# Performance work log

Measured on AMD Instinct MI355X. Metric: run time of the kernel, lower is better.

Reference implementation:

```python
import jax, jax.numpy as jnp
import numpy as np

DIM = 4096
DIM_OUTS = (4096, 4096, 4096)
R = 8
SCALE = 1.0  # alpha defaults to r -> alpha/r = 1


def setup_inputs() -> dict:
    key = jax.random.key(0)
    ks = jax.random.split(key, 1 + len(DIM_OUTS))
    x = jax.random.normal(ks[0], (4, 4096, DIM), dtype=jnp.float32)
    # A ~ randn, B ~ zeros per torch init; use small randn for B so grads/outputs are nontrivial? 
    # Faithful to module init: B = zeros. Keep zeros.
    As = [jax.random.normal(ks[1 + i], (DIM, R), dtype=jnp.float32) for i in range(len(DIM_OUTS))]
    Bs = [jnp.zeros((R, d), dtype=jnp.float32) for d in DIM_OUTS]
    return {
        "x": x,
        "A0": As[0], "B0": Bs[0],
        "A1": As[1], "B1": Bs[1],
        "A2": As[2], "B2": Bs[2],
    }


def reference(x, A0, B0, A1, B1, A2, B2):
    # Faithful math: x @ concat([A_i @ B_i * scale], axis=-1)
    # Efficient form: compute (x @ A_i) @ B_i * scale per LoRA, then concat.
    # Same Rs allow stacking into one batched low-rank chain.
    A = jnp.stack([A0, A1, A2])          # [L, dim, r]
    B = jnp.stack([B0, B1, B2])          # [L, r, dim_out]
    xa = jnp.einsum('bsd,ldr->lbsr', x, A)   # [L, B, S, r]
    out = jnp.einsum('lbsr,lro->lbso', xa, B) * SCALE  # [L, B, S, dim_out]
    # concat along last dim in lora order
    L, Bb, S, O = out.shape
    return jnp.moveaxis(out, 0, 2).reshape(Bb, S, L * O)
```

## Files before the change

### kernel.cpp

```cpp
#include <hip/hip_runtime.h>


#define DIM       4096
#define M_ROWS    16384
#define NLORA     3
#define RANK      8
#define NC        24
#define OUT_COLS  12288

#define KC             512
#define ROWS_PER_WAVE  4
#define ROWS_PER_BLOCK 16

__launch_bounds__(256, 2)
__global__ void lora_xa_kernel(const float* __restrict__ x,
                               const float* __restrict__ A0,
                               const float* __restrict__ A1,
                               const float* __restrict__ A2,
                               float* __restrict__ xa) {
  __shared__ float At[NC][KC];

  const int tid  = threadIdx.x;
  const int lane = tid & 63;
  const int wave = tid >> 6;
  const int row0 = blockIdx.x * ROWS_PER_BLOCK + wave * ROWS_PER_WAVE;

  float acc[ROWS_PER_WAVE][NC];
#pragma unroll
  for (int r = 0; r < ROWS_PER_WAVE; ++r)
#pragma unroll
    for (int c = 0; c < NC; ++c) acc[r][c] = 0.f;

  for (int kb = 0; kb < DIM; kb += KC) {
#pragma unroll
    for (int j = 0; j < 12; ++j) {
      const int l   = j >> 2;
      const int rem = tid + (j & 3) * 256;
      const int dof = rem >> 1;
      const int rq  = (rem & 1) * 4;
      const float* Ap = (l == 0) ? A0 : (l == 1) ? A1 : A2;
      const float4 v = *(const float4*)(Ap + (size_t)(kb + dof) * RANK + rq);
      At[l * RANK + rq + 0][dof] = v.x;
      At[l * RANK + rq + 1][dof] = v.y;
      At[l * RANK + rq + 2][dof] = v.z;
      At[l * RANK + rq + 3][dof] = v.w;
    }
    __syncthreads();

#pragma unroll
    for (int step = 0; step < KC / 256; ++step) {
      const int kl = step * 256 + 4 * lane;
      const int kq = kb + kl;
      float4 xv[ROWS_PER_WAVE];
#pragma unroll
      for (int r = 0; r < ROWS_PER_WAVE; ++r)
        xv[r] = *(const float4*)(x + (size_t)(row0 + r) * DIM + kq);
#pragma unroll
      for (int c = 0; c < NC; ++c) {
        const float4 av = *(const float4*)(&At[c][kl]);
#pragma unroll
        for (int r = 0; r < ROWS_PER_WAVE; ++r) {
          acc[r][c] = fmaf(xv[r].x, av.x, acc[r][c]);
          acc[r][c] = fmaf(xv[r].y, av.y, acc[r][c]);
          acc[r][c] = fmaf(xv[r].z, av.z, acc[r][c]);
          acc[r][c] = fmaf(xv[r].w, av.w, acc[r][c]);
        }
      }
    }
    __syncthreads();
  }

#pragma unroll
  for (int r = 0; r < ROWS_PER_WAVE; ++r)
#pragma unroll
    for (int c = 0; c < NC; ++c) {
      float v = acc[r][c];
#pragma unroll
      for (int off = 32; off > 0; off >>= 1) v += __shfl_xor(v, off, 64);
      acc[r][c] = v;
    }

  float outv[ROWS_PER_WAVE];
#pragma unroll
  for (int c = 0; c < NC; ++c)
#pragma unroll
    for (int r = 0; r < ROWS_PER_WAVE; ++r)
      if (lane == c) outv[r] = acc[r][c];

  if (lane < NC) {
#pragma unroll
    for (int r = 0; r < ROWS_PER_WAVE; ++r)
      xa[(size_t)(row0 + r) * NC + lane] = outv[r];
  }
}

#define ROW_TILE        128
#define COLS_PER_BLOCK  1024

__launch_bounds__(256, 4)
__global__ void lora_expand_kernel(const float* __restrict__ xa,
                                   const float* __restrict__ B0,
                                   const float* __restrict__ B1,
                                   const float* __restrict__ B2,
                                   float* __restrict__ out) {
  const int ctile = blockIdx.x;
  const int rtile = blockIdx.y;
  const int l     = ctile >> 2;
  const int o     = (ctile & 3) * COLS_PER_BLOCK + threadIdx.x * 4;
  const float* B  = (l == 0) ? B0 : (l == 1) ? B1 : B2;

  float4 b[RANK];
#pragma unroll
  for (int r = 0; r < RANK; ++r)
    b[r] = *(const float4*)(B + (size_t)r * DIM + o);

  const int row0    = rtile * ROW_TILE;
  const size_t ocol = (size_t)l * DIM + o;

  for (int i = 0; i < ROW_TILE; ++i) {
    const int row = row0 + i;
    const float* xr = xa + (size_t)row * NC + l * RANK;
    const float4 s0 = *(const float4*)(xr);
    const float4 s1 = *(const float4*)(xr + 4);
    const float s[8] = {s0.x, s0.y, s0.z, s0.w, s1.x, s1.y, s1.z, s1.w};

    float4 acc = {0.f, 0.f, 0.f, 0.f};
#pragma unroll
    for (int r = 0; r < RANK; ++r) {
      acc.x = fmaf(s[r], b[r].x, acc.x);
      acc.y = fmaf(s[r], b[r].y, acc.y);
      acc.z = fmaf(s[r], b[r].z, acc.z);
      acc.w = fmaf(s[r], b[r].w, acc.w);
    }
    *(float4*)(out + (size_t)row * OUT_COLS + ocol) = acc;
  }
}

extern "C" void kernel_launch(void* const* d_in, const int* in_sizes, int n_in,
                              void* d_out, int out_size, void* d_ws, size_t ws_size,
                              hipStream_t stream) {
  const float* x  = (const float*)d_in[0];
  const float* A0 = (const float*)d_in[1];
  const float* B0 = (const float*)d_in[2];
  const float* A1 = (const float*)d_in[3];
  const float* B1 = (const float*)d_in[4];
  const float* A2 = (const float*)d_in[5];
  const float* B2 = (const float*)d_in[6];
  float* out = (float*)d_out;
  float* xa  = (float*)d_ws;

  if (ws_size < (size_t)M_ROWS * NC * sizeof(float)) return;

  lora_xa_kernel<<<dim3(M_ROWS / ROWS_PER_BLOCK), dim3(256), 0, stream>>>(
      x, A0, A1, A2, xa);
  lora_expand_kernel<<<dim3(OUT_COLS / COLS_PER_BLOCK, M_ROWS / ROW_TILE),
                       dim3(256), 0, stream>>>(xa, B0, B1, B2, out);
}
```

Measured before the change: 1.164 ms.

## Fuse down-projection and up-projection into one kernel via shared-memory xa

Merges the x·A reduction kernel and the B expansion kernel into a single launch. Each block keeps its 16×24 xa tile in shared memory and writes all 12288 output columns for its rows, so the xa workspace round trip and the second launch go away. The K chunk also shrinks from 512 to 256, which halves the A staging in shared memory. In exchange, each block reloads the B fragments for its 16 rows, which adds B reads, and the output write phase now runs serially after the reduction inside each block.

```diff
diff --git a/kernel.cpp b/kernel.cpp
--- a/kernel.cpp
+++ b/kernel.cpp
@@ -3,27 +3,31 @@
 
 #define DIM       4096
 #define M_ROWS    16384
-#define NLORA     3
 #define RANK      8
 #define NC        24
 #define OUT_COLS  12288
 
-#define KC             512
+#define KC             256
 #define ROWS_PER_WAVE  4
 #define ROWS_PER_BLOCK 16
 
 __launch_bounds__(256, 2)
-__global__ void lora_xa_kernel(const float* __restrict__ x,
-                               const float* __restrict__ A0,
-                               const float* __restrict__ A1,
-                               const float* __restrict__ A2,
-                               float* __restrict__ xa) {
+__global__ void lora_fused_kernel(const float* __restrict__ x,
+                                  const float* __restrict__ A0,
+                                  const float* __restrict__ A1,
+                                  const float* __restrict__ A2,
+                                  const float* __restrict__ B0,
+                                  const float* __restrict__ B1,
+                                  const float* __restrict__ B2,
+                                  float* __restrict__ out) {
   __shared__ float At[NC][KC];
+  __shared__ float xa_s[ROWS_PER_BLOCK][NC];
 
-  const int tid  = threadIdx.x;
-  const int lane = tid & 63;
-  const int wave = tid >> 6;
-  const int row0 = blockIdx.x * ROWS_PER_BLOCK + wave * ROWS_PER_WAVE;
+  const int tid   = threadIdx.x;
+  const int lane  = tid & 63;
+  const int wave  = tid >> 6;
+  const int row0b = blockIdx.x * ROWS_PER_BLOCK;
+  const int row0  = row0b + wave * ROWS_PER_WAVE;
 
   float acc[ROWS_PER_WAVE][NC];
 #pragma unroll
@@ -33,11 +37,11 @@
 
   for (int kb = 0; kb < DIM; kb += KC) {
 #pragma unroll
-    for (int j = 0; j < 12; ++j) {
-      const int l   = j >> 2;
-      const int rem = tid + (j & 3) * 256;
-      const int dof = rem >> 1;
-      const int rq  = (rem & 1) * 4;
+    for (int j = 0; j < 6; ++j) {
+      const int l   = j >> 1;
+      const int idx = tid + (j & 1) * 256;
+      const int dof = idx >> 1;
+      const int rq  = (idx & 1) * 4;
       const float* Ap = (l == 0) ? A0 : (l == 1) ? A1 : A2;
       const float4 v = *(const float4*)(Ap + (size_t)(kb + dof) * RANK + rq);
       At[l * RANK + rq + 0][dof] = v.x;
@@ -47,24 +51,20 @@
     }
     __syncthreads();
 
+    const int kl = 4 * lane;
+    float4 xv[ROWS_PER_WAVE];
 #pragma unroll
-    for (int step = 0; step < KC / 256; ++step) {
-      const int kl = step * 256 + 4 * lane;
-      const int kq = kb + kl;
-      float4 xv[ROWS_PER_WAVE];
+    for (int r = 0; r < ROWS_PER_WAVE; ++r)
+      xv[r] = *(const float4*)(x + (size_t)(row0 + r) * DIM + kb + kl);
 #pragma unroll
-      for (int r = 0; r < ROWS_PER_WAVE; ++r)
-        xv[r] = *(const float4*)(x + (size_t)(row0 + r) * DIM + kq);
+    for (int c = 0; c < NC; ++c) {
+      const float4 av = *(const float4*)(&At[c][kl]);
 #pragma unroll
-      for (int c = 0; c < NC; ++c) {
-        const float4 av = *(const float4*)(&At[c][kl]);
-#pragma unroll
-        for (int r = 0; r < ROWS_PER_WAVE; ++r) {
-          acc[r][c] = fmaf(xv[r].x, av.x, acc[r][c]);
-          acc[r][c] = fmaf(xv[r].y, av.y, acc[r][c]);
-          acc[r][c] = fmaf(xv[r].z, av.z, acc[r][c]);
-          acc[r][c] = fmaf(xv[r].w, av.w, acc[r][c]);
-        }
+      for (int r = 0; r < ROWS_PER_WAVE; ++r) {
+        acc[r][c] = fmaf(xv[r].x, av.x, acc[r][c]);
+        acc[r][c] = fmaf(xv[r].y, av.y, acc[r][c]);
+        acc[r][c] = fmaf(xv[r].z, av.z, acc[r][c]);
+        acc[r][c] = fmaf(xv[r].w, av.w, acc[r][c]);
       }
     }
     __syncthreads();
@@ -90,49 +90,38 @@
   if (lane < NC) {
 #pragma unroll
     for (int r = 0; r < ROWS_PER_WAVE; ++r)
-      xa[(size_t)(row0 + r) * NC + lane] = outv[r];
+      xa_s[wave * ROWS_PER_WAVE + r][lane] = outv[r];
   }
-}
+  __syncthreads();
 
-#define ROW_TILE        128
-#define COLS_PER_BLOCK  1024
+#pragma unroll
+  for (int ct = 0; ct < 12; ++ct) {
+    const int l  = ct >> 2;
+    const int oc = ct * 1024 + tid * 4;
+    const int ob = oc - l * DIM;
+    const float* B = (l == 0) ? B0 : (l == 1) ? B1 : B2;
 
-__launch_bounds__(256, 4)
-__global__ void lora_expand_kernel(const float* __restrict__ xa,
-                                   const float* __restrict__ B0,
-                                   const float* __restrict__ B1,
-                                   const float* __restrict__ B2,
-                                   float* __restrict__ out) {
-  const int ctile = blockIdx.x;
-  const int rtile = blockIdx.y;
-  const int l     = ctile >> 2;
-  const int o     = (ctile & 3) * COLS_PER_BLOCK + threadIdx.x * 4;
-  const float* B  = (l == 0) ? B0 : (l == 1) ? B1 : B2;
+    float4 b[RANK];
+#pragma unroll
+    for (int r = 0; r < RANK; ++r)
+      b[r] = *(const float4*)(B + (size_t)r * DIM + ob);
 
-  float4 b[RANK];
+#pragma unroll 4
+    for (int i = 0; i < ROWS_PER_BLOCK; ++i) {
+      const float4 s0 = *(const float4*)(&xa_s[i][l * RANK]);
+      const float4 s1 = *(const float4*)(&xa_s[i][l * RANK + 4]);
+      const float s[8] = {s0.x, s0.y, s0.z, s0.w, s1.x, s1.y, s1.z, s1.w};
+
+      float4 av = {0.f, 0.f, 0.f, 0.f};
 #pragma unroll
-  for (int r = 0; r < RANK; ++r)
-    b[r] = *(const float4*)(B + (size_t)r * DIM + o);
-
-  const int row0    = rtile * ROW_TILE;
-  const size_t ocol = (size_t)l * DIM + o;
-
-  for (int i = 0; i < ROW_TILE; ++i) {
-    const int row = row0 + i;
-    const float* xr = xa + (size_t)row * NC + l * RANK;
-    const float4 s0 = *(const float4*)(xr);
-    const float4 s1 = *(const float4*)(xr + 4);
-    const float s[8] = {s0.x, s0.y, s0.z, s0.w, s1.x, s1.y, s1.z, s1.w};
-
-    float4 acc = {0.f, 0.f, 0.f, 0.f};
-#pragma unroll
-    for (int r = 0; r < RANK; ++r) {
-      acc.x = fmaf(s[r], b[r].x, acc.x);
-      acc.y = fmaf(s[r], b[r].y, acc.y);
-      acc.z = fmaf(s[r], b[r].z, acc.z);
-      acc.w = fmaf(s[r], b[r].w, acc.w);
+      for (int r = 0; r < RANK; ++r) {
+        av.x = fmaf(s[r], b[r].x, av.x);
+        av.y = fmaf(s[r], b[r].y, av.y);
+        av.z = fmaf(s[r], b[r].z, av.z);
+        av.w = fmaf(s[r], b[r].w, av.w);
+      }
+      *(float4*)(out + (size_t)(row0b + i) * OUT_COLS + oc) = av;
     }
-    *(float4*)(out + (size_t)row * OUT_COLS + ocol) = acc;
   }
 }
 
@@ -147,12 +136,7 @@
   const float* A2 = (const float*)d_in[5];
   const float* B2 = (const float*)d_in[6];
   float* out = (float*)d_out;
-  float* xa  = (float*)d_ws;
 
-  if (ws_size < (size_t)M_ROWS * NC * sizeof(float)) return;
-
-  lora_xa_kernel<<<dim3(M_ROWS / ROWS_PER_BLOCK), dim3(256), 0, stream>>>(
-      x, A0, A1, A2, xa);
-  lora_expand_kernel<<<dim3(OUT_COLS / COLS_PER_BLOCK, M_ROWS / ROW_TILE),
-                       dim3(256), 0, stream>>>(xa, B0, B1, B2, out);
+  lora_fused_kernel<<<dim3(M_ROWS / ROWS_PER_BLOCK), dim3(256), 0, stream>>>(
+      x, A0, A1, A2, B0, B1, B2, out);
 }
```

Measured after the change: 1.185 ms. No clear change (+1.8%).

## Prefetch x before A staging and stage xa rows in LDS for expand

Applied to the files above, without the earlier changes.

The xa kernel now issues all x loads for a K-chunk before staging A into shared memory, so global latency overlaps the A transpose. Its occupancy hint rises from 2 to 3 blocks, which may force register spills given the 96-float accumulator. The expand kernel doubles its row tile to 256, loads each block's xa slice into LDS once with one row per thread, and partially unrolls the store loop. This replaces repeated per-row global reads of xa with LDS broadcasts. Both kernels are bound by memory traffic (reading x, writing a large output), so the gain is likely small.

```diff
diff --git a/kernel.cpp b/kernel.cpp
--- a/kernel.cpp
+++ b/kernel.cpp
@@ -3,7 +3,6 @@
 
 #define DIM       4096
 #define M_ROWS    16384
-#define NLORA     3
 #define RANK      8
 #define NC        24
 #define OUT_COLS  12288
@@ -12,7 +11,7 @@
 #define ROWS_PER_WAVE  4
 #define ROWS_PER_BLOCK 16
 
-__launch_bounds__(256, 2)
+__launch_bounds__(256, 3)
 __global__ void lora_xa_kernel(const float* __restrict__ x,
                                const float* __restrict__ A0,
                                const float* __restrict__ A1,
@@ -32,12 +31,20 @@
     for (int c = 0; c < NC; ++c) acc[r][c] = 0.f;
 
   for (int kb = 0; kb < DIM; kb += KC) {
+    float4 xv[2][ROWS_PER_WAVE];
+#pragma unroll
+    for (int step = 0; step < 2; ++step)
+#pragma unroll
+      for (int r = 0; r < ROWS_PER_WAVE; ++r)
+        xv[step][r] = *(const float4*)(x + (size_t)(row0 + r) * DIM + kb +
+                                       step * 256 + 4 * lane);
+
 #pragma unroll
     for (int j = 0; j < 12; ++j) {
       const int l   = j >> 2;
-      const int rem = tid + (j & 3) * 256;
-      const int dof = rem >> 1;
-      const int rq  = (rem & 1) * 4;
+      const int idx = tid + (j & 3) * 256;
+      const int dof = idx >> 1;
+      const int rq  = (idx & 1) * 4;
       const float* Ap = (l == 0) ? A0 : (l == 1) ? A1 : A2;
       const float4 v = *(const float4*)(Ap + (size_t)(kb + dof) * RANK + rq);
       At[l * RANK + rq + 0][dof] = v.x;
@@ -48,22 +55,17 @@
     __syncthreads();
 
 #pragma unroll
-    for (int step = 0; step < KC / 256; ++step) {
+    for (int step = 0; step < 2; ++step) {
       const int kl = step * 256 + 4 * lane;
-      const int kq = kb + kl;
-      float4 xv[ROWS_PER_WAVE];
-#pragma unroll
-      for (int r = 0; r < ROWS_PER_WAVE; ++r)
-        xv[r] = *(const float4*)(x + (size_t)(row0 + r) * DIM + kq);
 #pragma unroll
       for (int c = 0; c < NC; ++c) {
         const float4 av = *(const float4*)(&At[c][kl]);
 #pragma unroll
         for (int r = 0; r < ROWS_PER_WAVE; ++r) {
-          acc[r][c] = fmaf(xv[r].x, av.x, acc[r][c]);
-          acc[r][c] = fmaf(xv[r].y, av.y, acc[r][c]);
-          acc[r][c] = fmaf(xv[r].z, av.z, acc[r][c]);
-          acc[r][c] = fmaf(xv[r].w, av.w, acc[r][c]);
+          acc[r][c] = fmaf(xv[step][r].x, av.x, acc[r][c]);
+          acc[r][c] = fmaf(xv[step][r].y, av.y, acc[r][c]);
+          acc[r][c] = fmaf(xv[step][r].z, av.z, acc[r][c]);
+          acc[r][c] = fmaf(xv[step][r].w, av.w, acc[r][c]);
         }
       }
     }
@@ -94,8 +96,7 @@
   }
 }
 
-#define ROW_TILE        128
-#define COLS_PER_BLOCK  1024
+#define ROW_TILE 256
 
 __launch_bounds__(256, 4)
 __global__ void lora_expand_kernel(const float* __restrict__ xa,
@@ -103,36 +104,46 @@
                                    const float* __restrict__ B1,
                                    const float* __restrict__ B2,
                                    float* __restrict__ out) {
+  __shared__ float xs[ROW_TILE][12];
+
+  const int tid   = threadIdx.x;
   const int ctile = blockIdx.x;
   const int rtile = blockIdx.y;
   const int l     = ctile >> 2;
-  const int o     = (ctile & 3) * COLS_PER_BLOCK + threadIdx.x * 4;
+  const int oc    = ctile * 1024 + tid * 4;
+  const int ob    = oc - l * DIM;
   const float* B  = (l == 0) ? B0 : (l == 1) ? B1 : B2;
+  const int row0  = rtile * ROW_TILE;
 
   float4 b[RANK];
 #pragma unroll
   for (int r = 0; r < RANK; ++r)
-    b[r] = *(const float4*)(B + (size_t)r * DIM + o);
+    b[r] = *(const float4*)(B + (size_t)r * DIM + ob);
 
-  const int row0    = rtile * ROW_TILE;
-  const size_t ocol = (size_t)l * DIM + o;
+  {
+    const float* src = xa + (size_t)(row0 + tid) * NC + l * RANK;
+    const float4 v0 = *(const float4*)(src);
+    const float4 v1 = *(const float4*)(src + 4);
+    *(float4*)(&xs[tid][0]) = v0;
+    *(float4*)(&xs[tid][4]) = v1;
+  }
+  __syncthreads();
 
+#pragma unroll 8
   for (int i = 0; i < ROW_TILE; ++i) {
-    const int row = row0 + i;
-    const float* xr = xa + (size_t)row * NC + l * RANK;
-    const float4 s0 = *(const float4*)(xr);
-    const float4 s1 = *(const float4*)(xr + 4);
+    const float4 s0 = *(const float4*)(&xs[i][0]);
+    const float4 s1 = *(const float4*)(&xs[i][4]);
     const float s[8] = {s0.x, s0.y, s0.z, s0.w, s1.x, s1.y, s1.z, s1.w};
 
-    float4 acc = {0.f, 0.f, 0.f, 0.f};
+    float4 av = {0.f, 0.f, 0.f, 0.f};
 #pragma unroll
     for (int r = 0; r < RANK; ++r) {
-      acc.x = fmaf(s[r], b[r].x, acc.x);
-      acc.y = fmaf(s[r], b[r].y, acc.y);
-      acc.z = fmaf(s[r], b[r].z, acc.z);
-      acc.w = fmaf(s[r], b[r].w, acc.w);
+      av.x = fmaf(s[r], b[r].x, av.x);
+      av.y = fmaf(s[r], b[r].y, av.y);
+      av.z = fmaf(s[r], b[r].z, av.z);
+      av.w = fmaf(s[r], b[r].w, av.w);
     }
-    *(float4*)(out + (size_t)row * OUT_COLS + ocol) = acc;
+    *(float4*)(out + (size_t)(row0 + i) * OUT_COLS + oc) = av;
   }
 }
 
@@ -153,6 +164,6 @@
 
   lora_xa_kernel<<<dim3(M_ROWS / ROWS_PER_BLOCK), dim3(256), 0, stream>>>(
       x, A0, A1, A2, xa);
-  lora_expand_kernel<<<dim3(OUT_COLS / COLS_PER_BLOCK, M_ROWS / ROW_TILE),
-                       dim3(256), 0, stream>>>(xa, B0, B1, B2, out);
+  lora_expand_kernel<<<dim3(12, M_ROWS / ROW_TILE), dim3(256), 0, stream>>>(
+      xa, B0, B1, B2, out);
 }
```

Result: slower. 1.272 ms (+9.3%).

## Prefetch x before A staging, shrink rows per wave, nontemporal output stores

Applied to the files above, without the earlier changes.

The first kernel now loads all x vectors for a K chunk before staging A into shared memory, so global loads overlap the LDS fill. Rows per wave drop from 4 to 2 and occupancy is raised to 3 blocks per CU, which doubles the number of blocks and the redundant A staging work. The expand kernel unrolls its row loop by 8 and writes the large output with nontemporal stores to avoid polluting the cache. Together these target memory latency in the reduction kernel and write bandwidth in the expand kernel.

```diff
diff --git a/kernel.cpp b/kernel.cpp
--- a/kernel.cpp
+++ b/kernel.cpp
@@ -3,16 +3,17 @@
 
 #define DIM       4096
 #define M_ROWS    16384
-#define NLORA     3
 #define RANK      8
 #define NC        24
 #define OUT_COLS  12288
 
+typedef float floatx4 __attribute__((ext_vector_type(4)));
+
 #define KC             512
-#define ROWS_PER_WAVE  4
-#define ROWS_PER_BLOCK 16
+#define ROWS_PER_WAVE  2
+#define ROWS_PER_BLOCK 8
 
-__launch_bounds__(256, 2)
+__launch_bounds__(256, 3)
 __global__ void lora_xa_kernel(const float* __restrict__ x,
                                const float* __restrict__ A0,
                                const float* __restrict__ A1,
@@ -32,12 +33,20 @@
     for (int c = 0; c < NC; ++c) acc[r][c] = 0.f;
 
   for (int kb = 0; kb < DIM; kb += KC) {
+    float4 xv[2][ROWS_PER_WAVE];
+#pragma unroll
+    for (int step = 0; step < 2; ++step)
+#pragma unroll
+      for (int r = 0; r < ROWS_PER_WAVE; ++r)
+        xv[step][r] = *(const float4*)(x + (size_t)(row0 + r) * DIM + kb +
+                                       step * 256 + 4 * lane);
+
 #pragma unroll
     for (int j = 0; j < 12; ++j) {
       const int l   = j >> 2;
-      const int rem = tid + (j & 3) * 256;
-      const int dof = rem >> 1;
-      const int rq  = (rem & 1) * 4;
+      const int idx = tid + (j & 3) * 256;
+      const int dof = idx >> 1;
+      const int rq  = (idx & 1) * 4;
       const float* Ap = (l == 0) ? A0 : (l == 1) ? A1 : A2;
       const float4 v = *(const float4*)(Ap + (size_t)(kb + dof) * RANK + rq);
       At[l * RANK + rq + 0][dof] = v.x;
@@ -48,22 +57,17 @@
     __syncthreads();
 
 #pragma unroll
-    for (int step = 0; step < KC / 256; ++step) {
+    for (int step = 0; step < 2; ++step) {
       const int kl = step * 256 + 4 * lane;
-      const int kq = kb + kl;
-      float4 xv[ROWS_PER_WAVE];
-#pragma unroll
-      for (int r = 0; r < ROWS_PER_WAVE; ++r)
-        xv[r] = *(const float4*)(x + (size_t)(row0 + r) * DIM + kq);
 #pragma unroll
       for (int c = 0; c < NC; ++c) {
         const float4 av = *(const float4*)(&At[c][kl]);
 #pragma unroll
         for (int r = 0; r < ROWS_PER_WAVE; ++r) {
-          acc[r][c] = fmaf(xv[r].x, av.x, acc[r][c]);
-          acc[r][c] = fmaf(xv[r].y, av.y, acc[r][c]);
-          acc[r][c] = fmaf(xv[r].z, av.z, acc[r][c]);
-          acc[r][c] = fmaf(xv[r].w, av.w, acc[r][c]);
+          acc[r][c] = fmaf(xv[step][r].x, av.x, acc[r][c]);
+          acc[r][c] = fmaf(xv[step][r].y, av.y, acc[r][c]);
+          acc[r][c] = fmaf(xv[step][r].z, av.z, acc[r][c]);
+          acc[r][c] = fmaf(xv[step][r].w, av.w, acc[r][c]);
         }
       }
     }
@@ -117,6 +121,7 @@
   const int row0    = rtile * ROW_TILE;
   const size_t ocol = (size_t)l * DIM + o;
 
+#pragma unroll 8
   for (int i = 0; i < ROW_TILE; ++i) {
     const int row = row0 + i;
     const float* xr = xa + (size_t)row * NC + l * RANK;
@@ -124,7 +129,7 @@
     const float4 s1 = *(const float4*)(xr + 4);
     const float s[8] = {s0.x, s0.y, s0.z, s0.w, s1.x, s1.y, s1.z, s1.w};
 
-    float4 acc = {0.f, 0.f, 0.f, 0.f};
+    floatx4 acc = {0.f, 0.f, 0.f, 0.f};
 #pragma unroll
     for (int r = 0; r < RANK; ++r) {
       acc.x = fmaf(s[r], b[r].x, acc.x);
@@ -132,7 +137,7 @@
       acc.z = fmaf(s[r], b[r].z, acc.z);
       acc.w = fmaf(s[r], b[r].w, acc.w);
     }
-    *(float4*)(out + (size_t)row * OUT_COLS + ocol) = acc;
+    __builtin_nontemporal_store(acc, (floatx4*)(out + (size_t)row * OUT_COLS + ocol));
   }
 }
 
@@ -153,6 +158,6 @@
 
   lora_xa_kernel<<<dim3(M_ROWS / ROWS_PER_BLOCK), dim3(256), 0, stream>>>(
       x, A0, A1, A2, xa);
-  lora_expand_kernel<<<dim3(OUT_COLS / COLS_PER_BLOCK, M_ROWS / ROW_TILE),
-                       dim3(256), 0, stream>>>(xa, B0, B1, B2, out);
+  lora_expand_kernel<<<dim3(12, M_ROWS / ROW_TILE), dim3(256), 0, stream>>>(
+      xa, B0, B1, B2, out);
 }
```

After: 1.086 ms. -6.7%, faster.
